# Kernel optimization log

Measured on AMD Instinct MI355X. Metric: run time of the kernel, lower is better.

## Reference

```python
import jax, jax.numpy as jnp
import numpy as np

N_NODES = 50000
N_EDGES = 800000
NODE_FEAT = 3
HID = 64
L = 4


def setup_inputs() -> dict:
    key = jax.random.key(0)
    ks = jax.random.split(key, 16)
    s = 0.05  # init scale
    inp = {
        'node_pos': jax.random.normal(ks[0], (N_NODES, 3), jnp.float32),
        'node_features': jax.random.normal(ks[1], (N_NODES, NODE_FEAT), jnp.float32),
        'edge_index': jax.random.randint(ks[2], (2, N_EDGES), 0, N_NODES, jnp.int64),
        # encoders
        'enc_w': jax.random.normal(ks[3], (NODE_FEAT, HID), jnp.float32) * s,
        'enc_b': jnp.zeros((HID,), jnp.float32),
        'edge_enc_w': jax.random.normal(ks[4], (3, HID), jnp.float32) * s,
        'edge_enc_b': jnp.zeros((HID,), jnp.float32),
        # stacked per-layer GNOLayer params
        'ew1': jax.random.normal(ks[5], (L, 3 * HID, HID), jnp.float32) * s,
        'eb1': jnp.zeros((L, HID), jnp.float32),
        'ew2': jax.random.normal(ks[6], (L, HID, HID), jnp.float32) * s,
        'eb2': jnp.zeros((L, HID), jnp.float32),
        'nw1': jax.random.normal(ks[7], (L, 2 * HID, HID), jnp.float32) * s,
        'nb1': jnp.zeros((L, HID), jnp.float32),
        'nw2': jax.random.normal(ks[8], (L, HID, HID), jnp.float32) * s,
        'nb2': jnp.zeros((L, HID), jnp.float32),
        # decoder
        'dec_w': jax.random.normal(ks[9], (HID, 1), jnp.float32) * s,
        'dec_b': jnp.zeros((1,), jnp.float32),
    }
    return inp


def reference(node_pos, node_features, edge_index, enc_w, enc_b, edge_enc_w,
              edge_enc_b, ew1, eb1, ew2, eb2, nw1, nb1, nw2, nb2, dec_w, dec_b):
    src, dst = edge_index[0], edge_index[1]
    edge_vec = node_pos[dst] - node_pos[src]            # [E, 3]
    h = node_features @ enc_w + enc_b                   # [N, H]
    e = edge_vec @ edge_enc_w + edge_enc_b              # [E, H]

    def layer(h, p):
        w1, b1, w2, b2, m1, c1, m2, c2 = p
        edge_in = jnp.concatenate([h[src], h[dst], e], axis=-1)   # [E, 3H]
        msg = jax.nn.relu(edge_in @ w1 + b1) @ w2 + b2            # [E, H]
        agg = jax.ops.segment_sum(msg, dst, num_segments=N_NODES)  # [N, H]
        node_in = jnp.concatenate([h, agg], axis=-1)              # [N, 2H]
        return jax.nn.relu(node_in @ m1 + c1) @ m2 + c2, None

    h, _ = jax.lax.scan(layer, h, (ew1, eb1, ew2, eb2, nw1, nb1, nw2, nb2))
    return h @ dec_w + dec_b                            # [N, 1]
```

## Files before the change

### kernel.cpp

```cpp
#include <hip/hip_runtime.h>

#define N_NODES 50000
#define N_EDGES 800000
#define HID 64
#define LAYERS 4
#define EP_NPB 28
#define EP_CAP 2048

typedef unsigned short u16;
typedef __attribute__((ext_vector_type(8))) __bf16 bf16x8;
typedef __attribute__((ext_vector_type(8))) unsigned short u16x8;
typedef __attribute__((ext_vector_type(4))) float f32x4;

__device__ __forceinline__ u16 f2bf(float f) {
  unsigned u = __builtin_bit_cast(unsigned, f);
  u += 0x7fffu + ((u >> 16) & 1u);
  return (u16)(u >> 16);
}
__device__ __forceinline__ float bf2f(u16 s) {
  return __builtin_bit_cast(float, ((unsigned)s) << 16);
}

__global__ __launch_bounds__(256) void init_kernel(
    const float* __restrict__ nf, const float* __restrict__ enc_w,
    const float* __restrict__ enc_b,
    const float* __restrict__ ew1, const float* __restrict__ eb1,
    const float* __restrict__ ew2, const float* __restrict__ eb2,
    const float* __restrict__ nw1, const float* __restrict__ nw2,
    const float* __restrict__ edge_enc_w, const float* __restrict__ edge_enc_b,
    u16* __restrict__ h, u16* W1abT, float* Wvx, float* b1x,
    u16* NB1T, float* bb2, u16* M2T, int* __restrict__ cnt) {
  const int T = gridDim.x * 256;
  int tid = blockIdx.x * 256 + threadIdx.x;
  for (int i = tid; i < N_NODES; i += T) cnt[i] = 0;
  {
    const int szA = LAYERS * 128 * 64, szV = LAYERS * 3 * 64, szB = LAYERS * 64;
    const int szN = LAYERS * 64 * 128, szb2 = LAYERS * 64, szM = LAYERS * 64 * 64;
    const int tot = szA + szV + szB + szN + szb2 + szM;
    for (int i = tid; i < tot; i += T) {
      int idx = i;
      if (idx < szA) {
        int l = idx / (128 * 64); int r = idx % (128 * 64);
        int nfc = r / 64; int k = r % 64;
        int half = nfc >> 6, f = nfc & 63;
        W1abT[idx] = f2bf(ew1[(l * 192 + half * 64 + k) * 64 + f]);
        continue;
      }
      idx -= szA;
      if (idx < szV) {
        int l = idx / 192, r = idx % 192, a = r / 64, f = r % 64;
        float s = 0.f;
        for (int m = 0; m < 64; ++m) s += edge_enc_w[a * 64 + m] * ew1[(l * 192 + 128 + m) * 64 + f];
        Wvx[idx] = s;
        continue;
      }
      idx -= szV;
      if (idx < szB) {
        int l = idx / 64, f = idx % 64;
        float s = eb1[l * 64 + f];
        for (int m = 0; m < 64; ++m) s += edge_enc_b[m] * ew1[(l * 192 + 128 + m) * 64 + f];
        b1x[idx] = s;
        continue;
      }
      idx -= szB;
      if (idx < szN) {
        int l = idx / 8192, r = idx % 8192, f = r / 128, k = r % 128;
        float v;
        if (k < 64) v = nw1[(l * 128 + k) * 64 + f];
        else {
          int j = k - 64; float s = 0.f;
          for (int g = 0; g < 64; ++g)
            s += ew2[(l * 64 + j) * 64 + g] * nw1[(l * 128 + 64 + g) * 64 + f];
          v = s;
        }
        NB1T[idx] = f2bf(v);
        continue;
      }
      idx -= szN;
      if (idx < szb2) {
        int l = idx / 64, f = idx % 64;
        float s = 0.f;
        for (int g = 0; g < 64; ++g) s += eb2[l * 64 + g] * nw1[(l * 128 + 64 + g) * 64 + f];
        bb2[idx] = s;
        continue;
      }
      idx -= szb2;
      int l = idx / 4096, r = idx % 4096, f = r / 64, k = r % 64;
      M2T[idx] = f2bf(nw2[(l * 64 + k) * 64 + f]);
    }
  }
  for (int i = tid; i < N_NODES * HID; i += T) {
    int n = i >> 6, j = i & 63;
    float s = enc_b[j]
            + nf[n * 3 + 0] * enc_w[j]
            + nf[n * 3 + 1] * enc_w[64 + j]
            + nf[n * 3 + 2] * enc_w[128 + j];
    h[i] = f2bf(s);
  }
}

__global__ __launch_bounds__(256) void hist_kernel(const int* __restrict__ dstA,
                                                   int* __restrict__ cnt,
                                                   int* __restrict__ rank) {
  int idx = blockIdx.x * 256 + threadIdx.x;
  if (idx < N_EDGES) rank[idx] = atomicAdd(&cnt[dstA[idx]], 1);
}

#define SCAN_NBLK 25
__global__ __launch_bounds__(256) void scan1_kernel(const int* __restrict__ cnt,
                                                    int* __restrict__ offs,
                                                    int* __restrict__ partials) {
  __shared__ int sm[2048];
  __shared__ int ws2[256];
  int t = threadIdx.x, b = blockIdx.x;
  int base = b * 2048;
#pragma unroll
  for (int i = 0; i < 8; ++i) {
    int idx = base + i * 256 + t;
    sm[i * 256 + t] = (idx < N_NODES) ? cnt[idx] : 0;
  }
  __syncthreads();
  int loc[8]; int s = 0;
#pragma unroll
  for (int i = 0; i < 8; ++i) { loc[i] = s; s += sm[t * 8 + i]; }
  ws2[t] = s;
  __syncthreads();
  for (int off = 1; off < 256; off <<= 1) {
    int u = (t >= off) ? ws2[t - off] : 0;
    __syncthreads();
    ws2[t] += u;
    __syncthreads();
  }
  int tbase = (t > 0) ? ws2[t - 1] : 0;
  if (t == 255) partials[b] = ws2[255];
#pragma unroll
  for (int i = 0; i < 8; ++i) {
    int idx = base + t * 8 + i;
    if (idx < N_NODES) offs[idx] = tbase + loc[i];
  }
}

__global__ __launch_bounds__(256) void scan3_kernel(int* __restrict__ offs,
                                                    const int* __restrict__ partials) {
  __shared__ int pref;
  int blk = (blockIdx.x * 256) >> 11;
  if (threadIdx.x == 0) {
    int s = 0;
    for (int i = 0; i < blk; ++i) s += partials[i];
    pref = s;
  }
  __syncthreads();
  int idx = blockIdx.x * 256 + threadIdx.x;
  if (idx < N_NODES) offs[idx] += pref;
}

__global__ __launch_bounds__(256) void scatter_kernel(const int* __restrict__ ei,
                                                      const int* __restrict__ offs,
                                                      const int* __restrict__ rank,
                                                      int* __restrict__ srcS64) {
  int idx = blockIdx.x * 256 + threadIdx.x;
  if (idx >= N_EDGES) return;
  int s = ei[idx], d = ei[N_EDGES + idx];
  srcS64[offs[d] + rank[idx]] = s << 6;
}

__global__ __launch_bounds__(256) void su_kernel(const u16* __restrict__ h,
                                                 const u16* __restrict__ W1abT,
                                                 const float* __restrict__ Wvx,
                                                 const float* __restrict__ b1x,
                                                 const float* __restrict__ pos,
                                                 u16* __restrict__ Sarr,
                                                 u16* __restrict__ Uarr, int layer) {
  __shared__ float sPos[192];
  int t = threadIdx.x;
  int lane = t & 63, wvi = t >> 6;
  int n16 = lane & 15, quad = lane >> 4;
  int n0 = blockIdx.x * 64;
  if (t < 192) {
    int idx = n0 * 3 + t;
    sPos[t] = (idx < N_NODES * 3) ? pos[idx] : 0.f;
  }
  __syncthreads();

  bf16x8 B[2][2];
  float w0[2], w1[2], w2[2], bb[2]; bool isU[2];
#pragma unroll
  for (int nt = 0; nt < 2; ++nt) {
    int col = wvi * 32 + nt * 16 + n16;
    const u16* p = W1abT + (size_t)(layer * 128 + col) * 64 + quad * 8;
    B[nt][0] = __builtin_bit_cast(bf16x8, *(const u16x8*)(p));
    B[nt][1] = __builtin_bit_cast(bf16x8, *(const u16x8*)(p + 32));
    int f = col & 63; isU[nt] = col >= 64;
    w0[nt] = Wvx[(layer * 3 + 0) * 64 + f];
    w1[nt] = Wvx[(layer * 3 + 1) * 64 + f];
    w2[nt] = Wvx[(layer * 3 + 2) * 64 + f];
    bb[nt] = b1x[layer * 64 + f];
  }
  f32x4 acc[4][2];
#pragma unroll
  for (int m = 0; m < 4; ++m)
#pragma unroll
    for (int nt = 0; nt < 2; ++nt) acc[m][nt] = (f32x4){0.f, 0.f, 0.f, 0.f};

#pragma unroll
  for (int m = 0; m < 4; ++m) {
    int row = n0 + m * 16 + n16;
    if (row >= N_NODES) row = N_NODES - 1;
    const u16* hp = h + (size_t)row * 64 + quad * 8;
    bf16x8 a0 = __builtin_bit_cast(bf16x8, *(const u16x8*)(hp));
    bf16x8 a1 = __builtin_bit_cast(bf16x8, *(const u16x8*)(hp + 32));
#pragma unroll
    for (int nt = 0; nt < 2; ++nt) {
      acc[m][nt] = __builtin_amdgcn_mfma_f32_16x16x32_bf16(a0, B[nt][0], acc[m][nt], 0, 0, 0);
      acc[m][nt] = __builtin_amdgcn_mfma_f32_16x16x32_bf16(a1, B[nt][1], acc[m][nt], 0, 0, 0);
    }
  }
#pragma unroll
  for (int m = 0; m < 4; ++m)
#pragma unroll
    for (int nt = 0; nt < 2; ++nt) {
      int col = wvi * 32 + nt * 16 + n16;
      int f = col & 63;
#pragma unroll
      for (int r = 0; r < 4; ++r) {
        int e = m * 16 + quad * 4 + r;
        int grow = n0 + e;
        if (grow < N_NODES) {
          float P = sPos[e * 3] * w0[nt] + sPos[e * 3 + 1] * w1[nt] + sPos[e * 3 + 2] * w2[nt];
          if (!isU[nt]) Sarr[(size_t)grow * 64 + f] = f2bf(acc[m][nt][r] - P);
          else          Uarr[(size_t)grow * 64 + f] = f2bf(acc[m][nt][r] + P + bb[nt]);
        }
      }
    }
}

__global__ __launch_bounds__(256) void ep_kernel(const u16* __restrict__ Sarr,
                                                 const u16* __restrict__ Uarr,
                                                 const int* __restrict__ srcS64,
                                                 const int* __restrict__ offs,
                                                 u16* __restrict__ aggH) {
  __shared__ int sIdx[EP_CAP];
  __shared__ int sOff[EP_NPB + 1];
  int t = threadIdx.x;
  int f = t & 63, wvi = t >> 6;
  int d0b = blockIdx.x * EP_NPB;
  if (t <= EP_NPB) {
    int d = d0b + t;
    sOff[t] = (d < N_NODES) ? offs[d] : N_EDGES;
  }
  __syncthreads();
  int eS = sOff[0];
  int nE = sOff[EP_NPB] - eS;
  bool fit = (nE <= EP_CAP);
  if (fit) {
    for (int i = t; i < nE; i += 256) sIdx[i] = srcS64[eS + i];
  }
  __syncthreads();

  for (int i = 0; i < 7; ++i) {
    int nl = wvi * 7 + i;
    int d = d0b + nl;
    if (d >= N_NODES) break;
    int e0 = sOff[nl];
    int deg = sOff[nl + 1] - e0;
    float Ub = bf2f(Uarr[(size_t)d * 64 + f]);
    float sum = 0.f;
    int full = deg & ~7;
    int base = 0;
    if (fit) {
      int rel = e0 - eS;
      for (; base < full; base += 8) {
        u16 S[8];
#pragma unroll
        for (int k = 0; k < 8; ++k) {
          int s64 = sIdx[rel + base + k];
          S[k] = Sarr[(size_t)s64 + f];
        }
#pragma unroll
        for (int k = 0; k < 8; ++k) sum += fmaxf(bf2f(S[k]) + Ub, 0.f);
      }
      if (base < deg) {
        u16 S[8]; bool ok[8];
#pragma unroll
        for (int k = 0; k < 8; ++k) {
          int j = base + k;
          ok[k] = j < deg;
          int s64 = sIdx[rel + (ok[k] ? j : 0)];
          S[k] = Sarr[(size_t)s64 + f];
        }
#pragma unroll
        for (int k = 0; k < 8; ++k) {
          float z = fmaxf(bf2f(S[k]) + Ub, 0.f);
          sum += ok[k] ? z : 0.f;
        }
      }
    } else {
      for (; base < full; base += 8) {
        u16 S[8];
#pragma unroll
        for (int k = 0; k < 8; ++k) {
          int s64 = srcS64[e0 + base + k];
          S[k] = Sarr[(size_t)s64 + f];
        }
#pragma unroll
        for (int k = 0; k < 8; ++k) sum += fmaxf(bf2f(S[k]) + Ub, 0.f);
      }
      if (base < deg) {
        u16 S[8]; bool ok[8];
#pragma unroll
        for (int k = 0; k < 8; ++k) {
          int j = base + k;
          ok[k] = j < deg;
          int s64 = srcS64[e0 + (ok[k] ? j : 0)];
          S[k] = Sarr[(size_t)s64 + f];
        }
#pragma unroll
        for (int k = 0; k < 8; ++k) {
          float z = fmaxf(bf2f(S[k]) + Ub, 0.f);
          sum += ok[k] ? z : 0.f;
        }
      }
    }
    aggH[(size_t)d * 64 + f] = f2bf(sum);
  }
}

__global__ __launch_bounds__(256) void node_kernel(
    const u16* __restrict__ h, const u16* __restrict__ aggH,
    const int* __restrict__ cnt,
    const u16* __restrict__ NB1T, const float* __restrict__ nb1,
    const float* __restrict__ bb2,
    const u16* __restrict__ M2T, const float* __restrict__ nb2,
    u16* __restrict__ h2, int layer,
    const u16* __restrict__ W1abT, const float* __restrict__ Wvx,
    const float* __restrict__ b1x, const float* __restrict__ pos,
    u16* __restrict__ Sarr, u16* __restrict__ Uarr,
    const float* __restrict__ dec_w, const float* __restrict__ dec_b,
    float* __restrict__ out) {
  __shared__ u16 Hs[64 * 72];
  __shared__ float sDeg[64];
  __shared__ float sPos[192];
  __shared__ float sRed[64][4];
  int t = threadIdx.x;
  int lane = t & 63, wvi = t >> 6;
  int n16 = lane & 15, quad = lane >> 4;
  int F = wvi * 16;
  int n0 = blockIdx.x * 64;

  if (t < 64) {
    int gn = n0 + t;
    sDeg[t] = (gn < N_NODES) ? (float)cnt[gn] : 0.f;
  }
  if (t >= 64 && t < 256) {
    int i = t - 64;
    int idx = n0 * 3 + i;
    sPos[i] = (idx < N_NODES * 3) ? pos[idx] : 0.f;
  }

  bf16x8 B1[4], B2[2];
  {
    const u16* p = NB1T + (size_t)(layer * 64 + F + n16) * 128 + quad * 8;
#pragma unroll
    for (int ks = 0; ks < 4; ++ks) B1[ks] = __builtin_bit_cast(bf16x8, *(const u16x8*)(p + ks * 32));
    const u16* q = M2T + (size_t)(layer * 64 + F + n16) * 64 + quad * 8;
#pragma unroll
    for (int ks = 0; ks < 2; ++ks) B2[ks] = __builtin_bit_cast(bf16x8, *(const u16x8*)(q + ks * 32));
  }
  float bias1 = nb1[layer * 64 + F + n16];
  float bb2f = bb2[layer * 64 + F + n16];
  float bias2 = nb2[layer * 64 + F + n16];
  __syncthreads();

  f32x4 acc[4];
#pragma unroll
  for (int m = 0; m < 4; ++m) acc[m] = (f32x4){0.f, 0.f, 0.f, 0.f};
#pragma unroll
  for (int m = 0; m < 4; ++m) {
    int row = n0 + m * 16 + n16;
    if (row >= N_NODES) row = N_NODES - 1;
    const u16* hp = h + (size_t)row * 64 + quad * 8;
    const u16* ap = aggH + (size_t)row * 64 + quad * 8;
    bf16x8 a0 = __builtin_bit_cast(bf16x8, *(const u16x8*)(hp));
    bf16x8 a1 = __builtin_bit_cast(bf16x8, *(const u16x8*)(hp + 32));
    bf16x8 a2 = __builtin_bit_cast(bf16x8, *(const u16x8*)(ap));
    bf16x8 a3 = __builtin_bit_cast(bf16x8, *(const u16x8*)(ap + 32));
    acc[m] = __builtin_amdgcn_mfma_f32_16x16x32_bf16(a0, B1[0], acc[m], 0, 0, 0);
    acc[m] = __builtin_amdgcn_mfma_f32_16x16x32_bf16(a1, B1[1], acc[m], 0, 0, 0);
    acc[m] = __builtin_amdgcn_mfma_f32_16x16x32_bf16(a2, B1[2], acc[m], 0, 0, 0);
    acc[m] = __builtin_amdgcn_mfma_f32_16x16x32_bf16(a3, B1[3], acc[m], 0, 0, 0);
  }
#pragma unroll
  for (int m = 0; m < 4; ++m)
#pragma unroll
    for (int r = 0; r < 4; ++r) {
      int e = m * 16 + quad * 4 + r;
      float v = acc[m][r] + bias1 + sDeg[e] * bb2f;
      v = v > 0.f ? v : 0.f;
      Hs[e * 72 + F + n16] = f2bf(v);
    }
  __syncthreads();

  float c2[4][4];
#pragma unroll
  for (int m = 0; m < 4; ++m) {
    const u16* hp = Hs + (m * 16 + n16) * 72 + quad * 8;
    f32x4 c = (f32x4){0.f, 0.f, 0.f, 0.f};
#pragma unroll
    for (int ks = 0; ks < 2; ++ks) {
      bf16x8 a = __builtin_bit_cast(bf16x8, *(const u16x8*)(hp + ks * 32));
      c = __builtin_amdgcn_mfma_f32_16x16x32_bf16(a, B2[ks], c, 0, 0, 0);
    }
#pragma unroll
    for (int r = 0; r < 4; ++r) c2[m][r] = c[r] + bias2;
  }
  __syncthreads();

#pragma unroll
  for (int m = 0; m < 4; ++m)
#pragma unroll
    for (int r = 0; r < 4; ++r) {
      int e = m * 16 + quad * 4 + r;
      u16 hv = f2bf(c2[m][r]);
      Hs[e * 72 + F + n16] = hv;
      int gn = n0 + e;
      if (layer < LAYERS - 1 && gn < N_NODES)
        h2[(size_t)gn * 64 + F + n16] = hv;
    }
  __syncthreads();

  if (layer < LAYERS - 1) {
    int lp = layer + 1;
    bf16x8 B3[2][2];
    float w0[2], w1[2], w2[2], bb[2]; bool isU[2];
#pragma unroll
    for (int nt = 0; nt < 2; ++nt) {
      int col = wvi * 32 + nt * 16 + n16;
      const u16* p = W1abT + (size_t)(lp * 128 + col) * 64 + quad * 8;
      B3[nt][0] = __builtin_bit_cast(bf16x8, *(const u16x8*)(p));
      B3[nt][1] = __builtin_bit_cast(bf16x8, *(const u16x8*)(p + 32));
      int f = col & 63; isU[nt] = col >= 64;
      w0[nt] = Wvx[(lp * 3 + 0) * 64 + f];
      w1[nt] = Wvx[(lp * 3 + 1) * 64 + f];
      w2[nt] = Wvx[(lp * 3 + 2) * 64 + f];
      bb[nt] = b1x[lp * 64 + f];
    }
    f32x4 a3[4][2];
#pragma unroll
    for (int m = 0; m < 4; ++m)
#pragma unroll
      for (int nt = 0; nt < 2; ++nt) a3[m][nt] = (f32x4){0.f, 0.f, 0.f, 0.f};
#pragma unroll
    for (int m = 0; m < 4; ++m) {
      const u16* hp = Hs + (m * 16 + n16) * 72 + quad * 8;
      bf16x8 a0 = __builtin_bit_cast(bf16x8, *(const u16x8*)(hp));
      bf16x8 a1 = __builtin_bit_cast(bf16x8, *(const u16x8*)(hp + 32));
#pragma unroll
      for (int nt = 0; nt < 2; ++nt) {
        a3[m][nt] = __builtin_amdgcn_mfma_f32_16x16x32_bf16(a0, B3[nt][0], a3[m][nt], 0, 0, 0);
        a3[m][nt] = __builtin_amdgcn_mfma_f32_16x16x32_bf16(a1, B3[nt][1], a3[m][nt], 0, 0, 0);
      }
    }
#pragma unroll
    for (int m = 0; m < 4; ++m)
#pragma unroll
      for (int nt = 0; nt < 2; ++nt) {
        int col = wvi * 32 + nt * 16 + n16;
        int f = col & 63;
#pragma unroll
        for (int r = 0; r < 4; ++r) {
          int e = m * 16 + quad * 4 + r;
          int grow = n0 + e;
          if (grow < N_NODES) {
            float P = sPos[e * 3] * w0[nt] + sPos[e * 3 + 1] * w1[nt] + sPos[e * 3 + 2] * w2[nt];
            if (!isU[nt]) Sarr[(size_t)grow * 64 + f] = f2bf(a3[m][nt][r] - P);
            else          Uarr[(size_t)grow * 64 + f] = f2bf(a3[m][nt][r] + P + bb[nt]);
          }
        }
      }
  } else {
    int e = t >> 2, part = t & 3;
    float s = 0.f;
#pragma unroll
    for (int j = 0; j < 16; ++j)
      s += bf2f(Hs[e * 72 + part * 16 + j]) * dec_w[part * 16 + j];
    sRed[e][part] = s;
    __syncthreads();
    if (part == 0) {
      int gn = n0 + e;
      if (gn < N_NODES)
        out[gn] = sRed[e][0] + sRed[e][1] + sRed[e][2] + sRed[e][3] + dec_b[0];
    }
  }
}

extern "C" void kernel_launch(void* const* d_in, const int* in_sizes, int n_in,
                              void* d_out, int out_size, void* d_ws, size_t ws_size,
                              hipStream_t stream) {
  const float* node_pos   = (const float*)d_in[0];
  const float* node_feat  = (const float*)d_in[1];
  const int*   edge_index = (const int*)d_in[2];
  const float* enc_w      = (const float*)d_in[3];
  const float* enc_b      = (const float*)d_in[4];
  const float* edge_enc_w = (const float*)d_in[5];
  const float* edge_enc_b = (const float*)d_in[6];
  const float* ew1        = (const float*)d_in[7];
  const float* eb1        = (const float*)d_in[8];
  const float* ew2        = (const float*)d_in[9];
  const float* eb2        = (const float*)d_in[10];
  const float* nw1        = (const float*)d_in[11];
  const float* nb1        = (const float*)d_in[12];
  const float* nw2        = (const float*)d_in[13];
  const float* nb2        = (const float*)d_in[14];
  const float* dec_w      = (const float*)d_in[15];
  const float* dec_b      = (const float*)d_in[16];
  float* out = (float*)d_out;

  char* ws = (char*)d_ws;
  size_t off = 0;
  u16*    hA    = (u16*)(ws + off);    off += (size_t)N_NODES * 64 * 2;
  u16*    hB    = (u16*)(ws + off);    off += (size_t)N_NODES * 64 * 2;
  u16*    Sarr  = (u16*)(ws + off);    off += (size_t)N_NODES * 64 * 2;
  u16*    Uarr  = (u16*)(ws + off);    off += (size_t)N_NODES * 64 * 2;
  u16*    aggH  = (u16*)(ws + off);    off += (size_t)N_NODES * 64 * 2;
  u16*    W1abT = (u16*)(ws + off);    off += (size_t)LAYERS * 128 * 64 * 2;
  float*  Wvx   = (float*)(ws + off);  off += (size_t)LAYERS * 3 * 64 * 4;
  float*  b1x   = (float*)(ws + off);  off += (size_t)LAYERS * 64 * 4;
  u16*    NB1T  = (u16*)(ws + off);    off += (size_t)LAYERS * 64 * 128 * 2;
  float*  bb2   = (float*)(ws + off);  off += (size_t)LAYERS * 64 * 4;
  u16*    M2T   = (u16*)(ws + off);    off += (size_t)LAYERS * 64 * 64 * 2;
  int*    cnt      = (int*)(ws + off); off += (size_t)N_NODES * 4;
  int*    offsB    = (int*)(ws + off); off += (size_t)N_NODES * 4;
  int*    partials = (int*)(ws + off); off += 32 * 4;
  int*    rank     = (int*)(ws + off); off += (size_t)N_EDGES * 4;
  int*    srcS64   = (int*)(ws + off); off += (size_t)N_EDGES * 4;

  const int* dstA = edge_index + N_EDGES;
  const int NBLK = (N_NODES + 63) / 64;
  const int EP_GRID = (N_NODES + EP_NPB - 1) / EP_NPB;

  init_kernel<<<1024, 256, 0, stream>>>(
      node_feat, enc_w, enc_b, ew1, eb1, ew2, eb2, nw1, nw2,
      edge_enc_w, edge_enc_b, hA, W1abT, Wvx, b1x, NB1T, bb2, M2T, cnt);

  hist_kernel<<<(N_EDGES + 255) / 256, 256, 0, stream>>>(dstA, cnt, rank);
  scan1_kernel<<<SCAN_NBLK, 256, 0, stream>>>(cnt, offsB, partials);
  scan3_kernel<<<(N_NODES + 255) / 256, 256, 0, stream>>>(offsB, partials);
  scatter_kernel<<<(N_EDGES + 255) / 256, 256, 0, stream>>>(edge_index, offsB, rank, srcS64);

  su_kernel<<<NBLK, 256, 0, stream>>>(hA, W1abT, Wvx, b1x, node_pos, Sarr, Uarr, 0);

  u16* hcur = hA; u16* hnext = hB;
  for (int l = 0; l < LAYERS; ++l) {
    ep_kernel<<<EP_GRID, 256, 0, stream>>>(Sarr, Uarr, srcS64, offsB, aggH);
    node_kernel<<<NBLK, 256, 0, stream>>>(hcur, aggH, cnt, NB1T, nb1, bb2, M2T, nb2,
                                          hnext, l, W1abT, Wvx, b1x, node_pos,
                                          Sarr, Uarr, dec_w, dec_b, out);
    u16* tmp = hcur; hcur = hnext; hnext = tmp;
  }
}
```

Baseline: 346.6 us.

## Fuse edge aggregation into node kernel with double-buffered S/U arrays

Removes the separate edge-pass kernel and performs the gather-relu-sum aggregation inside node_kernel, writing the aggregate into shared memory (aggT) instead of a global aggH buffer. S/U arrays are double-buffered because the fused kernel reads the previous layer's S/U while writing the next. The gather now has each lane load two bf16 features at once, with the two wave halves splitting edges and combining through a shuffle. Encoder init is also vectorised to write 8 bf16 values per store. This saves a launch and the aggH round trip per layer, but raises shared memory per block (which may lower occupancy) and puts the irregular gather work into the 64-node blocks.

Result: slower. 401.2 us (+15.7%).

```diff
diff --git a/kernel.cpp b/kernel.cpp
--- a/kernel.cpp
+++ b/kernel.cpp
@@ -4,7 +4,6 @@
 #define N_EDGES 800000
 #define HID 64
 #define LAYERS 4
-#define EP_NPB 28
 #define EP_CAP 2048
 
 typedef unsigned short u16;
@@ -89,13 +88,17 @@
       M2T[idx] = f2bf(nw2[(l * 64 + k) * 64 + f]);
     }
   }
-  for (int i = tid; i < N_NODES * HID; i += T) {
-    int n = i >> 6, j = i & 63;
-    float s = enc_b[j]
-            + nf[n * 3 + 0] * enc_w[j]
-            + nf[n * 3 + 1] * enc_w[64 + j]
-            + nf[n * 3 + 2] * enc_w[128 + j];
-    h[i] = f2bf(s);
+  for (int i = tid; i < N_NODES * 8; i += T) {
+    int n = i >> 3, j0 = (i & 7) * 8;
+    float x0 = nf[n * 3 + 0], x1 = nf[n * 3 + 1], x2 = nf[n * 3 + 2];
+    u16x8 v;
+#pragma unroll
+    for (int j = 0; j < 8; ++j) {
+      int jj = j0 + j;
+      float s = enc_b[jj] + x0 * enc_w[jj] + x1 * enc_w[64 + jj] + x2 * enc_w[128 + jj];
+      v[j] = f2bf(s);
+    }
+    *(u16x8*)(h + (size_t)n * 64 + j0) = v;
   }
 }
 
@@ -234,110 +237,23 @@
     }
 }
 
-__global__ __launch_bounds__(256) void ep_kernel(const u16* __restrict__ Sarr,
-                                                 const u16* __restrict__ Uarr,
-                                                 const int* __restrict__ srcS64,
-                                                 const int* __restrict__ offs,
-                                                 u16* __restrict__ aggH) {
-  __shared__ int sIdx[EP_CAP];
-  __shared__ int sOff[EP_NPB + 1];
-  int t = threadIdx.x;
-  int f = t & 63, wvi = t >> 6;
-  int d0b = blockIdx.x * EP_NPB;
-  if (t <= EP_NPB) {
-    int d = d0b + t;
-    sOff[t] = (d < N_NODES) ? offs[d] : N_EDGES;
-  }
-  __syncthreads();
-  int eS = sOff[0];
-  int nE = sOff[EP_NPB] - eS;
-  bool fit = (nE <= EP_CAP);
-  if (fit) {
-    for (int i = t; i < nE; i += 256) sIdx[i] = srcS64[eS + i];
-  }
-  __syncthreads();
-
-  for (int i = 0; i < 7; ++i) {
-    int nl = wvi * 7 + i;
-    int d = d0b + nl;
-    if (d >= N_NODES) break;
-    int e0 = sOff[nl];
-    int deg = sOff[nl + 1] - e0;
-    float Ub = bf2f(Uarr[(size_t)d * 64 + f]);
-    float sum = 0.f;
-    int full = deg & ~7;
-    int base = 0;
-    if (fit) {
-      int rel = e0 - eS;
-      for (; base < full; base += 8) {
-        u16 S[8];
-#pragma unroll
-        for (int k = 0; k < 8; ++k) {
-          int s64 = sIdx[rel + base + k];
-          S[k] = Sarr[(size_t)s64 + f];
-        }
-#pragma unroll
-        for (int k = 0; k < 8; ++k) sum += fmaxf(bf2f(S[k]) + Ub, 0.f);
-      }
-      if (base < deg) {
-        u16 S[8]; bool ok[8];
-#pragma unroll
-        for (int k = 0; k < 8; ++k) {
-          int j = base + k;
-          ok[k] = j < deg;
-          int s64 = sIdx[rel + (ok[k] ? j : 0)];
-          S[k] = Sarr[(size_t)s64 + f];
-        }
-#pragma unroll
-        for (int k = 0; k < 8; ++k) {
-          float z = fmaxf(bf2f(S[k]) + Ub, 0.f);
-          sum += ok[k] ? z : 0.f;
-        }
-      }
-    } else {
-      for (; base < full; base += 8) {
-        u16 S[8];
-#pragma unroll
-        for (int k = 0; k < 8; ++k) {
-          int s64 = srcS64[e0 + base + k];
-          S[k] = Sarr[(size_t)s64 + f];
-        }
-#pragma unroll
-        for (int k = 0; k < 8; ++k) sum += fmaxf(bf2f(S[k]) + Ub, 0.f);
-      }
-      if (base < deg) {
-        u16 S[8]; bool ok[8];
-#pragma unroll
-        for (int k = 0; k < 8; ++k) {
-          int j = base + k;
-          ok[k] = j < deg;
-          int s64 = srcS64[e0 + (ok[k] ? j : 0)];
-          S[k] = Sarr[(size_t)s64 + f];
-        }
-#pragma unroll
-        for (int k = 0; k < 8; ++k) {
-          float z = fmaxf(bf2f(S[k]) + Ub, 0.f);
-          sum += ok[k] ? z : 0.f;
-        }
-      }
-    }
-    aggH[(size_t)d * 64 + f] = f2bf(sum);
-  }
-}
-
 __global__ __launch_bounds__(256) void node_kernel(
-    const u16* __restrict__ h, const u16* __restrict__ aggH,
-    const int* __restrict__ cnt,
+    const u16* __restrict__ h, const int* __restrict__ srcS64,
+    const int* __restrict__ offs,
     const u16* __restrict__ NB1T, const float* __restrict__ nb1,
     const float* __restrict__ bb2,
     const u16* __restrict__ M2T, const float* __restrict__ nb2,
     u16* __restrict__ h2, int layer,
     const u16* __restrict__ W1abT, const float* __restrict__ Wvx,
     const float* __restrict__ b1x, const float* __restrict__ pos,
-    u16* __restrict__ Sarr, u16* __restrict__ Uarr,
+    const u16* __restrict__ Sr, const u16* __restrict__ Ur,
+    u16* __restrict__ Sw, u16* __restrict__ Uw,
     const float* __restrict__ dec_w, const float* __restrict__ dec_b,
     float* __restrict__ out) {
   __shared__ u16 Hs[64 * 72];
+  __shared__ u16 aggT[64 * 72];
+  __shared__ int sIdx[EP_CAP];
+  __shared__ int sOff[65];
   __shared__ float sDeg[64];
   __shared__ float sPos[192];
   __shared__ float sRed[64][4];
@@ -347,15 +263,113 @@
   int F = wvi * 16;
   int n0 = blockIdx.x * 64;
 
-  if (t < 64) {
-    int gn = n0 + t;
-    sDeg[t] = (gn < N_NODES) ? (float)cnt[gn] : 0.f;
-  }
+  if (t <= 64) {
+    int d = n0 + t;
+    sOff[t] = (d < N_NODES) ? offs[d] : N_EDGES;
+  }
+  __syncthreads();
+  if (t < 64) sDeg[t] = (float)(sOff[t + 1] - sOff[t]);
   if (t >= 64 && t < 256) {
     int i = t - 64;
     int idx = n0 * 3 + i;
     sPos[i] = (idx < N_NODES * 3) ? pos[idx] : 0.f;
   }
+  int eS = sOff[0];
+  int nE = sOff[64] - eS;
+  bool fit = (nE <= EP_CAP);
+  if (fit) {
+    for (int i = t; i < nE; i += 256) sIdx[i] = srcS64[eS + i];
+  }
+  __syncthreads();
+
+  {
+    int c = lane & 31, half = lane >> 5;
+    size_t cb = (size_t)(c << 2);
+    const char* Sb = (const char*)Sr;
+    for (int nl = 0; nl < 16; ++nl) {
+      int ln = wvi * 16 + nl;
+      int d = n0 + ln;
+      int dU = (d < N_NODES) ? d : (N_NODES - 1);
+      int e0 = sOff[ln];
+      int deg = sOff[ln + 1] - e0;
+      unsigned ub2 = *(const unsigned*)((const char*)Ur + (size_t)dU * 128 + cb);
+      float ua = bf2f((u16)(ub2 & 0xffffu));
+      float ub = bf2f((u16)(ub2 >> 16));
+      float suma = 0.f, sumb = 0.f;
+      int rel = e0 - eS;
+      int pf = (deg >> 1) & ~7;
+      if (fit) {
+        for (int base = 0; base < pf; base += 8) {
+          unsigned w[8];
+#pragma unroll
+          for (int k = 0; k < 8; ++k) {
+            int s64 = sIdx[rel + 2 * (base + k) + half];
+            w[k] = *(const unsigned*)(Sb + ((size_t)s64 << 1) + cb);
+          }
+#pragma unroll
+          for (int k = 0; k < 8; ++k) {
+            suma += fmaxf(bf2f((u16)(w[k] & 0xffffu)) + ua, 0.f);
+            sumb += fmaxf(bf2f((u16)(w[k] >> 16)) + ub, 0.f);
+          }
+        }
+        if (2 * pf < deg) {
+          unsigned w[8]; bool ok[8];
+#pragma unroll
+          for (int k = 0; k < 8; ++k) {
+            int j = 2 * (pf + k) + half;
+            ok[k] = j < deg;
+            int s64 = sIdx[rel + (ok[k] ? j : 0)];
+            w[k] = *(const unsigned*)(Sb + ((size_t)s64 << 1) + cb);
+          }
+#pragma unroll
+          for (int k = 0; k < 8; ++k) {
+            float za = fmaxf(bf2f((u16)(w[k] & 0xffffu)) + ua, 0.f);
+            float zb = fmaxf(bf2f((u16)(w[k] >> 16)) + ub, 0.f);
+            suma += ok[k] ? za : 0.f;
+            sumb += ok[k] ? zb : 0.f;
+          }
+        }
+      } else {
+        for (int base = 0; base < pf; base += 8) {
+          unsigned w[8];
+#pragma unroll
+          for (int k = 0; k < 8; ++k) {
+            int s64 = srcS64[e0 + 2 * (base + k) + half];
+            w[k] = *(const unsigned*)(Sb + ((size_t)s64 << 1) + cb);
+          }
+#pragma unroll
+          for (int k = 0; k < 8; ++k) {
+            suma += fmaxf(bf2f((u16)(w[k] & 0xffffu)) + ua, 0.f);
+            sumb += fmaxf(bf2f((u16)(w[k] >> 16)) + ub, 0.f);
+          }
+        }
+        if (2 * pf < deg) {
+          unsigned w[8]; bool ok[8];
+#pragma unroll
+          for (int k = 0; k < 8; ++k) {
+            int j = 2 * (pf + k) + half;
+            ok[k] = j < deg;
+            int s64 = srcS64[e0 + (ok[k] ? j : 0)];
+            w[k] = *(const unsigned*)(Sb + ((size_t)s64 << 1) + cb);
+          }
+#pragma unroll
+          for (int k = 0; k < 8; ++k) {
+            float za = fmaxf(bf2f((u16)(w[k] & 0xffffu)) + ua, 0.f);
+            float zb = fmaxf(bf2f((u16)(w[k] >> 16)) + ub, 0.f);
+            suma += ok[k] ? za : 0.f;
+            sumb += ok[k] ? zb : 0.f;
+          }
+        }
+      }
+      suma += __shfl_xor(suma, 32);
+      sumb += __shfl_xor(sumb, 32);
+      if (half == 0) {
+        unsigned pk = (unsigned)f2bf(suma) | ((unsigned)f2bf(sumb) << 16);
+        *(unsigned*)((char*)aggT + (size_t)ln * 144 + cb) = pk;
+      }
+    }
+  }
+  __syncthreads();
 
   bf16x8 B1[4], B2[2];
   {
@@ -369,7 +383,6 @@
   float bias1 = nb1[layer * 64 + F + n16];
   float bb2f = bb2[layer * 64 + F + n16];
   float bias2 = nb2[layer * 64 + F + n16];
-  __syncthreads();
 
   f32x4 acc[4];
 #pragma unroll
@@ -379,7 +392,7 @@
     int row = n0 + m * 16 + n16;
     if (row >= N_NODES) row = N_NODES - 1;
     const u16* hp = h + (size_t)row * 64 + quad * 8;
-    const u16* ap = aggH + (size_t)row * 64 + quad * 8;
+    const u16* ap = aggT + (m * 16 + n16) * 72 + quad * 8;
     bf16x8 a0 = __builtin_bit_cast(bf16x8, *(const u16x8*)(hp));
     bf16x8 a1 = __builtin_bit_cast(bf16x8, *(const u16x8*)(hp + 32));
     bf16x8 a2 = __builtin_bit_cast(bf16x8, *(const u16x8*)(ap));
@@ -472,8 +485,8 @@
           int grow = n0 + e;
           if (grow < N_NODES) {
             float P = sPos[e * 3] * w0[nt] + sPos[e * 3 + 1] * w1[nt] + sPos[e * 3 + 2] * w2[nt];
-            if (!isU[nt]) Sarr[(size_t)grow * 64 + f] = f2bf(a3[m][nt][r] - P);
-            else          Uarr[(size_t)grow * 64 + f] = f2bf(a3[m][nt][r] + P + bb[nt]);
+            if (!isU[nt]) Sw[(size_t)grow * 64 + f] = f2bf(a3[m][nt][r] - P);
+            else          Uw[(size_t)grow * 64 + f] = f2bf(a3[m][nt][r] + P + bb[nt]);
           }
         }
       }
@@ -519,9 +532,10 @@
   size_t off = 0;
   u16*    hA    = (u16*)(ws + off);    off += (size_t)N_NODES * 64 * 2;
   u16*    hB    = (u16*)(ws + off);    off += (size_t)N_NODES * 64 * 2;
-  u16*    Sarr  = (u16*)(ws + off);    off += (size_t)N_NODES * 64 * 2;
-  u16*    Uarr  = (u16*)(ws + off);    off += (size_t)N_NODES * 64 * 2;
-  u16*    aggH  = (u16*)(ws + off);    off += (size_t)N_NODES * 64 * 2;
+  u16*    Sarr0 = (u16*)(ws + off);    off += (size_t)N_NODES * 64 * 2;
+  u16*    Uarr0 = (u16*)(ws + off);    off += (size_t)N_NODES * 64 * 2;
+  u16*    Sarr1 = (u16*)(ws + off);    off += (size_t)N_NODES * 64 * 2;
+  u16*    Uarr1 = (u16*)(ws + off);    off += (size_t)N_NODES * 64 * 2;
   u16*    W1abT = (u16*)(ws + off);    off += (size_t)LAYERS * 128 * 64 * 2;
   float*  Wvx   = (float*)(ws + off);  off += (size_t)LAYERS * 3 * 64 * 4;
   float*  b1x   = (float*)(ws + off);  off += (size_t)LAYERS * 64 * 4;
@@ -536,7 +550,6 @@
 
   const int* dstA = edge_index + N_EDGES;
   const int NBLK = (N_NODES + 63) / 64;
-  const int EP_GRID = (N_NODES + EP_NPB - 1) / EP_NPB;
 
   init_kernel<<<1024, 256, 0, stream>>>(
       node_feat, enc_w, enc_b, ew1, eb1, ew2, eb2, nw1, nw2,
@@ -547,14 +560,17 @@
   scan3_kernel<<<(N_NODES + 255) / 256, 256, 0, stream>>>(offsB, partials);
   scatter_kernel<<<(N_EDGES + 255) / 256, 256, 0, stream>>>(edge_index, offsB, rank, srcS64);
 
-  su_kernel<<<NBLK, 256, 0, stream>>>(hA, W1abT, Wvx, b1x, node_pos, Sarr, Uarr, 0);
+  su_kernel<<<NBLK, 256, 0, stream>>>(hA, W1abT, Wvx, b1x, node_pos, Sarr0, Uarr0, 0);
 
   u16* hcur = hA; u16* hnext = hB;
+  u16* Sr = Sarr0; u16* Ur = Uarr0; u16* Sw = Sarr1; u16* Uw = Uarr1;
   for (int l = 0; l < LAYERS; ++l) {
-    ep_kernel<<<EP_GRID, 256, 0, stream>>>(Sarr, Uarr, srcS64, offsB, aggH);
-    node_kernel<<<NBLK, 256, 0, stream>>>(hcur, aggH, cnt, NB1T, nb1, bb2, M2T, nb2,
+    node_kernel<<<NBLK, 256, 0, stream>>>(hcur, srcS64, offsB, NB1T, nb1, bb2, M2T, nb2,
                                           hnext, l, W1abT, Wvx, b1x, node_pos,
-                                          Sarr, Uarr, dec_w, dec_b, out);
-    u16* tmp = hcur; hcur = hnext; hnext = tmp;
-  }
-}
+                                          Sr, Ur, Sw, Uw, dec_w, dec_b, out);
+    u16* tmp;
+    tmp = hcur; hcur = hnext; hnext = tmp;
+    tmp = Sr; Sr = Sw; Sw = tmp;
+    tmp = Ur; Ur = Uw; Uw = tmp;
+  }
+}
```

## Restructure edge gather to use 32-bit paired-feature loads and two destinations per wave

Applied to the files above, without the earlier changes.

The edge aggregation kernel now has each lane load two bf16 features as one 32-bit word. The two half-waves split a node's edges by parity and are combined with a cross-lane shuffle, and each wave processes two destination nodes at once for more loads in flight. Source indices are stored as byte offsets (s<<7), and nodes per block rise from 28 to 32. The init encoder loop also writes 8 bf16 values per store. This aims to raise memory-level parallelism in the latency-bound gather, at the cost of predicated wasted loads when the two nodes' degrees differ and extra registers.

Measured after the change: 356.4 us. 2.8% more time.

```diff
diff --git a/kernel.cpp b/kernel.cpp
--- a/kernel.cpp
+++ b/kernel.cpp
@@ -4,7 +4,7 @@
 #define N_EDGES 800000
 #define HID 64
 #define LAYERS 4
-#define EP_NPB 28
+#define EP_NPB 32
 #define EP_CAP 2048
 
 typedef unsigned short u16;
@@ -89,13 +89,17 @@
       M2T[idx] = f2bf(nw2[(l * 64 + k) * 64 + f]);
     }
   }
-  for (int i = tid; i < N_NODES * HID; i += T) {
-    int n = i >> 6, j = i & 63;
-    float s = enc_b[j]
-            + nf[n * 3 + 0] * enc_w[j]
-            + nf[n * 3 + 1] * enc_w[64 + j]
-            + nf[n * 3 + 2] * enc_w[128 + j];
-    h[i] = f2bf(s);
+  for (int i = tid; i < N_NODES * 8; i += T) {
+    int n = i >> 3, j0 = (i & 7) * 8;
+    float x0 = nf[n * 3 + 0], x1 = nf[n * 3 + 1], x2 = nf[n * 3 + 2];
+    u16x8 v;
+#pragma unroll
+    for (int j = 0; j < 8; ++j) {
+      int jj = j0 + j;
+      float s = enc_b[jj] + x0 * enc_w[jj] + x1 * enc_w[64 + jj] + x2 * enc_w[128 + jj];
+      v[j] = f2bf(s);
+    }
+    *(u16x8*)(h + (size_t)n * 64 + j0) = v;
   }
 }
 
@@ -157,11 +161,11 @@
 __global__ __launch_bounds__(256) void scatter_kernel(const int* __restrict__ ei,
                                                       const int* __restrict__ offs,
                                                       const int* __restrict__ rank,
-                                                      int* __restrict__ srcS64) {
+                                                      int* __restrict__ srcB) {
   int idx = blockIdx.x * 256 + threadIdx.x;
   if (idx >= N_EDGES) return;
   int s = ei[idx], d = ei[N_EDGES + idx];
-  srcS64[offs[d] + rank[idx]] = s << 6;
+  srcB[offs[d] + rank[idx]] = s << 7;
 }
 
 __global__ __launch_bounds__(256) void su_kernel(const u16* __restrict__ h,
@@ -236,13 +240,15 @@
 
 __global__ __launch_bounds__(256) void ep_kernel(const u16* __restrict__ Sarr,
                                                  const u16* __restrict__ Uarr,
-                                                 const int* __restrict__ srcS64,
+                                                 const int* __restrict__ srcB,
                                                  const int* __restrict__ offs,
                                                  u16* __restrict__ aggH) {
   __shared__ int sIdx[EP_CAP];
   __shared__ int sOff[EP_NPB + 1];
   int t = threadIdx.x;
-  int f = t & 63, wvi = t >> 6;
+  int lane = t & 63, wvi = t >> 6;
+  int c = lane & 31, half = lane >> 5;
+  size_t cb = (size_t)(c << 2);
   int d0b = blockIdx.x * EP_NPB;
   if (t <= EP_NPB) {
     int d = d0b + t;
@@ -253,75 +259,96 @@
   int nE = sOff[EP_NPB] - eS;
   bool fit = (nE <= EP_CAP);
   if (fit) {
-    for (int i = t; i < nE; i += 256) sIdx[i] = srcS64[eS + i];
-  }
-  __syncthreads();
-
-  for (int i = 0; i < 7; ++i) {
-    int nl = wvi * 7 + i;
-    int d = d0b + nl;
-    if (d >= N_NODES) break;
-    int e0 = sOff[nl];
-    int deg = sOff[nl + 1] - e0;
-    float Ub = bf2f(Uarr[(size_t)d * 64 + f]);
-    float sum = 0.f;
-    int full = deg & ~7;
-    int base = 0;
+    for (int i = t; i < nE; i += 256) sIdx[i] = srcB[eS + i];
+    if (t == 0 && nE < EP_CAP) sIdx[nE] = 0;
+  }
+  __syncthreads();
+
+  const char* Sb = (const char*)Sarr;
+  const char* Ub = (const char*)Uarr;
+  for (int i = 0; i < 8; i += 2) {
+    int lnA = wvi * 8 + i, lnB = lnA + 1;
+    int dA = d0b + lnA, dB = d0b + lnB;
+    int e0A = sOff[lnA], degA = sOff[lnA + 1] - e0A;
+    int e0B = sOff[lnB], degB = sOff[lnB + 1] - e0B;
+    int dAc = dA < N_NODES ? dA : N_NODES - 1;
+    int dBc = dB < N_NODES ? dB : N_NODES - 1;
+    unsigned upA = *(const unsigned*)(Ub + (size_t)dAc * 128 + cb);
+    unsigned upB = *(const unsigned*)(Ub + (size_t)dBc * 128 + cb);
+    float uaA = bf2f((u16)(upA & 0xffffu)), ubA = bf2f((u16)(upA >> 16));
+    float uaB = bf2f((u16)(upB & 0xffffu)), ubB = bf2f((u16)(upB >> 16));
+    float saA = 0.f, sbA = 0.f, saB = 0.f, sbB = 0.f;
+    int relA = (degA > 0) ? (e0A - eS) : 0;
+    int relB = (degB > 0) ? (e0B - eS) : 0;
+    int g0A = (degA > 0) ? e0A : 0;
+    int g0B = (degB > 0) ? e0B : 0;
+    int rA = (degA + 15) >> 4, rB = (degB + 15) >> 4;
+    int rmax = rA > rB ? rA : rB;
     if (fit) {
-      int rel = e0 - eS;
-      for (; base < full; base += 8) {
-        u16 S[8];
+      for (int r = 0; r < rmax; ++r) {
+        int base = r * 16 + half;
+        unsigned wA[8], wB[8]; bool okA[8], okB[8];
 #pragma unroll
         for (int k = 0; k < 8; ++k) {
-          int s64 = sIdx[rel + base + k];
-          S[k] = Sarr[(size_t)s64 + f];
-        }
-#pragma unroll
-        for (int k = 0; k < 8; ++k) sum += fmaxf(bf2f(S[k]) + Ub, 0.f);
-      }
-      if (base < deg) {
-        u16 S[8]; bool ok[8];
+          int j = base + 2 * k;
+          okA[k] = j < degA;
+          int sA = sIdx[relA + (okA[k] ? j : 0)];
+          wA[k] = *(const unsigned*)(Sb + (size_t)(unsigned)sA + cb);
+          okB[k] = j < degB;
+          int sB = sIdx[relB + (okB[k] ? j : 0)];
+          wB[k] = *(const unsigned*)(Sb + (size_t)(unsigned)sB + cb);
+        }
 #pragma unroll
         for (int k = 0; k < 8; ++k) {
-          int j = base + k;
-          ok[k] = j < deg;
-          int s64 = sIdx[rel + (ok[k] ? j : 0)];
-          S[k] = Sarr[(size_t)s64 + f];
-        }
+          float zaA = fmaxf(bf2f((u16)(wA[k] & 0xffffu)) + uaA, 0.f);
+          float zbA = fmaxf(bf2f((u16)(wA[k] >> 16)) + ubA, 0.f);
+          saA += okA[k] ? zaA : 0.f;
+          sbA += okA[k] ? zbA : 0.f;
+          float zaB = fmaxf(bf2f((u16)(wB[k] & 0xffffu)) + uaB, 0.f);
+          float zbB = fmaxf(bf2f((u16)(wB[k] >> 16)) + ubB, 0.f);
+          saB += okB[k] ? zaB : 0.f;
+          sbB += okB[k] ? zbB : 0.f;
+        }
+      }
+    } else {
+      for (int r = 0; r < rmax; ++r) {
+        int base = r * 16 + half;
+        unsigned wA[8], wB[8]; bool okA[8], okB[8];
 #pragma unroll
         for (int k = 0; k < 8; ++k) {
-          float z = fmaxf(bf2f(S[k]) + Ub, 0.f);
-          sum += ok[k] ? z : 0.f;
-        }
-      }
-    } else {
-      for (; base < full; base += 8) {
-        u16 S[8];
+          int j = base + 2 * k;
+          okA[k] = j < degA;
+          int sA = srcB[g0A + (okA[k] ? j : 0)];
+          wA[k] = *(const unsigned*)(Sb + (size_t)(unsigned)sA + cb);
+          okB[k] = j < degB;
+          int sB = srcB[g0B + (okB[k] ? j : 0)];
+          wB[k] = *(const unsigned*)(Sb + (size_t)(unsigned)sB + cb);
+        }
 #pragma unroll
         for (int k = 0; k < 8; ++k) {
-          int s64 = srcS64[e0 + base + k];
-          S[k] = Sarr[(size_t)s64 + f];
-        }
-#pragma unroll
-        for (int k = 0; k < 8; ++k) sum += fmaxf(bf2f(S[k]) + Ub, 0.f);
-      }
-      if (base < deg) {
-        u16 S[8]; bool ok[8];
-#pragma unroll
-        for (int k = 0; k < 8; ++k) {
-          int j = base + k;
-          ok[k] = j < deg;
-          int s64 = srcS64[e0 + (ok[k] ? j : 0)];
-          S[k] = Sarr[(size_t)s64 + f];
-        }
-#pragma unroll
-        for (int k = 0; k < 8; ++k) {
-          float z = fmaxf(bf2f(S[k]) + Ub, 0.f);
-          sum += ok[k] ? z : 0.f;
-        }
-      }
-    }
-    aggH[(size_t)d * 64 + f] = f2bf(sum);
+          float zaA = fmaxf(bf2f((u16)(wA[k] & 0xffffu)) + uaA, 0.f);
+          float zbA = fmaxf(bf2f((u16)(wA[k] >> 16)) + ubA, 0.f);
+          saA += okA[k] ? zaA : 0.f;
+          sbA += okA[k] ? zbA : 0.f;
+          float zaB = fmaxf(bf2f((u16)(wB[k] & 0xffffu)) + uaB, 0.f);
+          float zbB = fmaxf(bf2f((u16)(wB[k] >> 16)) + ubB, 0.f);
+          saB += okB[k] ? zaB : 0.f;
+          sbB += okB[k] ? zbB : 0.f;
+        }
+      }
+    }
+    saA += __shfl_xor(saA, 32);  sbA += __shfl_xor(sbA, 32);
+    saB += __shfl_xor(saB, 32);  sbB += __shfl_xor(sbB, 32);
+    if (half == 0) {
+      if (dA < N_NODES) {
+        unsigned pk = (unsigned)f2bf(saA) | ((unsigned)f2bf(sbA) << 16);
+        *(unsigned*)((char*)aggH + (size_t)dA * 128 + cb) = pk;
+      }
+      if (dB < N_NODES) {
+        unsigned pk = (unsigned)f2bf(saB) | ((unsigned)f2bf(sbB) << 16);
+        *(unsigned*)((char*)aggH + (size_t)dB * 128 + cb) = pk;
+      }
+    }
   }
 }
 
@@ -532,7 +559,7 @@
   int*    offsB    = (int*)(ws + off); off += (size_t)N_NODES * 4;
   int*    partials = (int*)(ws + off); off += 32 * 4;
   int*    rank     = (int*)(ws + off); off += (size_t)N_EDGES * 4;
-  int*    srcS64   = (int*)(ws + off); off += (size_t)N_EDGES * 4;
+  int*    srcB     = (int*)(ws + off); off += (size_t)N_EDGES * 4;
 
   const int* dstA = edge_index + N_EDGES;
   const int NBLK = (N_NODES + 63) / 64;
@@ -545,13 +572,13 @@
   hist_kernel<<<(N_EDGES + 255) / 256, 256, 0, stream>>>(dstA, cnt, rank);
   scan1_kernel<<<SCAN_NBLK, 256, 0, stream>>>(cnt, offsB, partials);
   scan3_kernel<<<(N_NODES + 255) / 256, 256, 0, stream>>>(offsB, partials);
-  scatter_kernel<<<(N_EDGES + 255) / 256, 256, 0, stream>>>(edge_index, offsB, rank, srcS64);
+  scatter_kernel<<<(N_EDGES + 255) / 256, 256, 0, stream>>>(edge_index, offsB, rank, srcB);
 
   su_kernel<<<NBLK, 256, 0, stream>>>(hA, W1abT, Wvx, b1x, node_pos, Sarr, Uarr, 0);
 
   u16* hcur = hA; u16* hnext = hB;
   for (int l = 0; l < LAYERS; ++l) {
-    ep_kernel<<<EP_GRID, 256, 0, stream>>>(Sarr, Uarr, srcS64, offsB, aggH);
+    ep_kernel<<<EP_GRID, 256, 0, stream>>>(Sarr, Uarr, srcB, offsB, aggH);
     node_kernel<<<NBLK, 256, 0, stream>>>(hcur, aggH, cnt, NB1T, nb1, bb2, M2T, nb2,
                                           hnext, l, W1abT, Wvx, b1x, node_pos,
                                           Sarr, Uarr, dec_w, dec_b, out);
```
